# Performance work log

Hardware: AMD Instinct MI355X
Metric: run time of the kernel (lower is better)

## Reference

```python
import jax, jax.numpy as jnp
import numpy as np

B, C, H, W = 4, 128, 128, 128
E, K, HID = 11, 6, 512  # num_experts, active_experts, 4*dim


def setup_inputs() -> dict:
    key = jax.random.key(0)
    ks = jax.random.split(key, 5)
    return {
        "x": jax.random.normal(ks[0], (B, C, H, W), jnp.float32),
        "gate_w": jax.random.normal(ks[1], (E, C), jnp.float32) * 0.02,
        "gate_b": jnp.zeros((E,), jnp.float32),
        "w1": jax.random.normal(ks[2], (E, HID, C), jnp.float32) * 0.02,
        "b1": jnp.zeros((E, HID), jnp.float32),
        "w2": jax.random.normal(ks[3], (E, C, HID), jnp.float32) * 0.02,
        "b2": jnp.zeros((E, C), jnp.float32),
    }


def reference(x, gate_w, gate_b, w1, b1, w2, b2):
    n_experts = gate_w.shape[0]
    k = K  # active_experts
    # channels-last for per-pixel routing / 1x1-conv-as-matmul
    xcl = jnp.transpose(x, (0, 2, 3, 1))  # [B,H,W,C]
    # --- router (1x1 conv gate + softmax over experts + top-k) ---
    logits = jnp.einsum('bhwc,ec->bhwe', xcl, gate_w) + gate_b
    scores = jax.nn.softmax(logits, axis=-1)            # [B,H,W,E]
    topk_p, topk_i = jax.lax.top_k(scores, k)           # [B,H,W,K]
    topk_p = topk_p / topk_p.sum(axis=-1, keepdims=True)
    # scatter routing weights into dense per-expert mask (indices distinct)
    onehot = jax.nn.one_hot(topk_i, n_experts, dtype=x.dtype)  # [B,H,W,K,E]
    mask = jnp.einsum('bhwke,bhwk->bhwe', onehot, topk_p)      # [B,H,W,E]
    # --- dense expert compute, masked accumulate (as in original loop) ---
    acc = jnp.zeros_like(xcl)
    for e in range(n_experts):
        h = jax.nn.gelu(jnp.einsum('bhwc,dc->bhwd', xcl, w1[e]) + b1[e],
                        approximate=False)  # torch GELU is exact erf form
        oe = jnp.einsum('bhwd,cd->bhwc', h, w2[e]) + b2[e]
        acc = acc + mask[..., e:e + 1] * oe
    y = x + jnp.transpose(acc, (0, 3, 1, 2))  # back to NCHW
    # --- load-balancing aux loss ---
    mean_prob = scores.mean(axis=(0, 1, 2))            # [E]
    mean_load = onehot.sum(axis=3).mean(axis=(0, 1, 2))  # binary mask mean, [E]
    aux_loss = n_experts * jnp.sum(mean_prob * mean_load)
    return (y, aux_loss)
```

## Files before the change

kernel.cpp:

```cpp
#include <hip/hip_runtime.h>
#include <stdint.h>

#define C_   128
#define HW_  16384
#define CHW_ (C_*HW_)
#define N_   65536
#define E_   11
#define K_   6
#define HID_ 512

typedef __attribute__((ext_vector_type(8))) _Float16 half8;
typedef __attribute__((ext_vector_type(2))) _Float16 h2;
typedef __attribute__((ext_vector_type(2))) __fp16 fp16v2;
typedef __attribute__((ext_vector_type(16))) float float16v;
typedef __attribute__((ext_vector_type(2))) unsigned uint2v;

#define GLD(g, s) __builtin_amdgcn_global_load_lds( \
    (const __attribute__((address_space(1))) unsigned int*)(uintptr_t)(g), \
    (__attribute__((address_space(3))) unsigned int*)(unsigned int)(uintptr_t)(s), 16, 0, 0)

__device__ __forceinline__ h2 pkrtz(float a, float b){
  union { fp16v2 f; h2 h; } u;
  u.f = __builtin_amdgcn_cvt_pkrtz(a, b);
  return u.h;
}
__device__ __forceinline__ h2 gelu2h(h2 v, h2 wr2){
  h2 u = v * v;
  h2 s = u * (h2)(_Float16)(-0.00076957f) + (h2)(_Float16)(0.0147811f);
  s = s * u + (h2)(_Float16)(-0.126434f);
  s = s * u + (h2)(_Float16)(0.795742f);
  h2 p = v * s;
  h2 phi = p * (h2)(_Float16)(0.5f) + (h2)(_Float16)(0.5f);
  return v * wr2 * phi;
}
__device__ __forceinline__ void pswap32(unsigned &a, unsigned &b){
#if __has_builtin(__builtin_amdgcn_permlane32_swap)
  uint2v r = __builtin_amdgcn_permlane32_swap(a, b, false, false);
  a = r.x; b = r.y;
#else
  asm volatile("v_permlane32_swap_b32 %0, %1" : "+v"(a), "+v"(b));
#endif
}

__global__ __launch_bounds__(256) void k_prep(const float* __restrict__ x,
                                              const float* __restrict__ gw,
                                              const float* __restrict__ gb,
                                              const float* __restrict__ w1,
                                              const float* __restrict__ w2,
                                              const float* __restrict__ b1,
                                              unsigned short* __restrict__ xcl,
                                              float* __restrict__ mask,
                                              unsigned short* __restrict__ wimg,
                                              unsigned short* __restrict__ b1h,
                                              float* __restrict__ part){
  __shared__ __align__(16) float tt[64 * 130];
  __shared__ __align__(16) float g[E_ * C_];
  __shared__ float gbs[E_];
  __shared__ float ap[E_], al[E_];

  if (blockIdx.x < 726){
    int t = blockIdx.x * 256 + threadIdx.x;
    if (t >= 185856) return;
    if (t >= 180224){
      int t2 = t - 180224;
      int rec = t2 >> 5, j5 = t2 & 31;
      int hi = j5 >> 4, j = j5 & 15;
      int e = rec >> 4, hc = rec & 15;
      int row = (j & 3) + 8 * (j >> 2) + 4 * hi;
      union { _Float16 h; unsigned short u; } cv;
      cv.h = (_Float16)b1[e * 512 + hc * 32 + row];
      b1h[rec * 32 + j5] = cv.u;
      return;
    }
    const float* src;
    size_t dst;
    if (t < 90112){
      int e = t >> 13, hid = (t >> 4) & 511, c8 = t & 15;
      src = w1 + (size_t)t * 8;
      int rec = e * 16 + (hid >> 5);
      int kc = c8 >> 1, half = c8 & 1;
      int l = (hid & 31) | (half << 5);
      dst = (size_t)rec * 8192 + kc * 512 + l * 8;
    } else {
      int u = t - 90112;
      int e = u >> 13, cc = (u >> 6) & 127, hd8 = u & 63;
      src = w2 + (size_t)u * 8;
      int rec = e * 16 + (hd8 >> 2);
      int kc2 = (hd8 >> 1) & 1, half = hd8 & 1, ct = cc >> 5;
      int l = (cc & 31) | (half << 5);
      dst = (size_t)rec * 8192 + 4096 + (ct * 2 + kc2) * 512 + l * 8;
    }
    float4 a = *(const float4*)src, b = *(const float4*)(src + 4);
    union { _Float16 h[8]; uint4 v; } u4;
    u4.h[0] = (_Float16)a.x; u4.h[1] = (_Float16)a.y;
    u4.h[2] = (_Float16)a.z; u4.h[3] = (_Float16)a.w;
    u4.h[4] = (_Float16)b.x; u4.h[5] = (_Float16)b.y;
    u4.h[6] = (_Float16)b.z; u4.h[7] = (_Float16)b.w;
    *(uint4*)(wimg + dst) = u4.v;
    return;
  }

  int tid = threadIdx.x;
  int pb = blockIdx.x - 726;
  int pix0 = pb * 64;
  int b = pix0 >> 14, hw0 = pix0 & 16383;
  const float* xb = x + (size_t)b * CHW_ + hw0;

  for (int i = tid; i < E_ * C_; i += 256) g[i] = gw[i];
  if (tid < E_) { gbs[tid] = gb[tid]; ap[tid] = 0.f; al[tid] = 0.f; }

  #pragma unroll 4
  for (int it = 0; it < 32; ++it){
    int flat = it * 256 + tid;
    int c = flat >> 6, p = flat & 63;
    tt[p * 130 + c] = xb[c * HW_ + p];
  }
  __syncthreads();
  #pragma unroll 4
  for (int it = 0; it < 16; ++it){
    int u = it * 256 + tid;
    int p = u >> 6, cc = u & 63;
    float f0 = tt[p * 130 + 2 * cc], f1 = tt[p * 130 + 2 * cc + 1];
    union { h2 h; unsigned u; } pv;
    pv.h = pkrtz(f0, f1);
    ((unsigned*)xcl)[(size_t)(pix0 + p) * 64 + cc] = pv.u;
  }

  int p = tid >> 2, t4 = tid & 3;
  float lg[E_];
  #pragma unroll
  for (int e = 0; e < E_; ++e) lg[e] = (t4 == 0) ? gbs[e] : 0.f;
  const float2* ttrow = (const float2*)(tt + p * 130 + t4 * 32);
  #pragma unroll 4
  for (int j2 = 0; j2 < 16; ++j2){
    float2 xv = ttrow[j2];
    #pragma unroll
    for (int e = 0; e < E_; ++e){
      float2 gv = *(const float2*)(g + e * C_ + t4 * 32 + j2 * 2);
      lg[e] = fmaf(xv.x, gv.x, lg[e]);
      lg[e] = fmaf(xv.y, gv.y, lg[e]);
    }
  }
  #pragma unroll
  for (int e = 0; e < E_; ++e){
    lg[e] += __shfl_xor(lg[e], 1, 64);
    lg[e] += __shfl_xor(lg[e], 2, 64);
  }
  float mx = lg[0];
  #pragma unroll
  for (int e = 1; e < E_; ++e) mx = fmaxf(mx, lg[e]);
  float pr[E_]; float s = 0.f;
  #pragma unroll
  for (int e = 0; e < E_; ++e){ pr[e] = expf(lg[e] - mx); s += pr[e]; }
  float inv = 1.0f / s;
  #pragma unroll
  for (int e = 0; e < E_; ++e) pr[e] *= inv;

  unsigned selmask = 0; float wsum = 0.f;
  for (int k = 0; k < K_; ++k){
    float bv = -1.f; int bi = 0;
    #pragma unroll
    for (int e = 0; e < E_; ++e){
      bool better = (((selmask >> e) & 1u) == 0u) && (pr[e] > bv);
      bv = better ? pr[e] : bv;
      bi = better ? e : bi;
    }
    selmask |= 1u << bi; wsum += bv;
  }
  float invw = 1.0f / wsum;
  if (t4 == 0){
    int pix = pix0 + p;
    #pragma unroll
    for (int e = 0; e < E_; ++e){
      bool sel = (selmask >> e) & 1u;
      mask[(size_t)pix * E_ + e] = sel ? pr[e] * invw : 0.f;
      atomicAdd(&ap[e], pr[e]);
      if (sel) atomicAdd(&al[e], 1.0f);
    }
  }
  __syncthreads();
  if (tid < E_){
    part[tid * 1024 + pb]        = ap[tid];
    part[(E_ + tid) * 1024 + pb] = al[tid];
  }
}

__global__ __launch_bounds__(512, 2) void k_ffn(const unsigned short* __restrict__ xcl,
                                                const unsigned short* __restrict__ wimg,
                                                const unsigned short* __restrict__ b1h,
                                                const float* __restrict__ b2,
                                                const float* __restrict__ mask,
                                                const float* __restrict__ aux,
                                                const float* __restrict__ x,
                                                float* __restrict__ y){
  __shared__ unsigned char smem[65536];
  __shared__ int b2f;
  int tid = threadIdx.x;
  int w = tid >> 6, l = tid & 63;
  int l31 = l & 31, hi = l >> 5;
  int hi4 = hi * 4;
  int pix0 = blockIdx.x * 256;
  int off = (blockIdx.x % 11) * 16;
  const unsigned char* wimgB = (const unsigned char*)wimg;
  const unsigned char* b1hB  = (const unsigned char*)b1h;

  if (tid == 0) b2f = 0;

  if (blockIdx.x == 0 && w == 0){
    float s = 0.f;
    const float invN = 1.0f / (float)N_;
    for (int e = 0; e < E_; ++e){
      float pa = 0.f, pl = 0.f;
      #pragma unroll
      for (int i = 0; i < 16; ++i){
        pa += aux[e * 1024 + i * 64 + l];
        pl += aux[(E_ + e) * 1024 + i * 64 + l];
      }
      #pragma unroll
      for (int o = 32; o; o >>= 1){
        pa += __shfl_down(pa, o);
        pl += __shfl_down(pl, o);
      }
      if (l == 0) s += (pa * invN) * (pl * invN);
    }
    if (l == 0) y[(size_t)N_ * C_] = (float)E_ * s;
  }

  half8 Xf[8];
  {
    const unsigned short* xrow = xcl + ((size_t)(pix0 + w * 32 + l31) << 7) + hi * 8;
    #pragma unroll
    for (int kc = 0; kc < 8; ++kc)
      Xf[kc] = *(const half8*)(xrow + kc * 16);
  }

  uint4 bhA[4], bhB[4];
  const size_t mrow = (size_t)(pix0 + w * 32 + l31) * 11;

  {
    #pragma unroll
    for (int k = 0; k < 2; ++k){
      int rec = off + k;
      const unsigned char* gs = wimgB + (size_t)rec * 16384 + w * 2048 + l * 16;
      unsigned char* dst = smem + k * 16384 + w * 2048;
      GLD(gs, dst);
      GLD(gs + 1024, dst + 1024);
    }
    #pragma unroll
    for (int k = 0; k < 2; ++k){
      const unsigned char* bp = b1hB + (off + k) * 64 + hi * 32;
      bhA[2 * k]     = *(const uint4*)(bp);
      bhA[2 * k + 1] = *(const uint4*)(bp + 16);
    }
  }
  float wrn = mask[mrow + (off >> 4)];
  __syncthreads();

  float16v facc[4];
  #pragma unroll
  for (int ct = 0; ct < 4; ++ct) facc[ct] = (float16v)0.0f;
  h2 wr2 = (h2)(_Float16)0.0f;

#define REC_BODY(WB, BH0, BH1)                                                      \
  {                                                                                 \
    float16v hacc_ = (float16v)0.0f;                                                \
    _Pragma("unroll")                                                               \
    for (int kc_ = 0; kc_ < 8; ++kc_){                                              \
      half8 a_ = *(const half8*)((WB) + kc_ * 1024 + l * 16);                       \
      hacc_ = __builtin_amdgcn_mfma_f32_32x32x16_f16(a_, Xf[kc_], hacc_, 0, 0, 0);  \
    }                                                                               \
    union { uint4 v[2]; h2 h[8]; } bu_;                                             \
    bu_.v[0] = BH0; bu_.v[1] = BH1;                                                 \
    unsigned pd_[8];                                                                \
    _Pragma("unroll")                                                               \
    for (int k_ = 0; k_ < 8; ++k_){                                                 \
      h2 v_ = pkrtz(hacc_[2 * k_], hacc_[2 * k_ + 1]);                              \
      v_ = v_ + bu_.h[k_];                                                          \
      union { h2 h; unsigned u; } g_;                                               \
      g_.h = gelu2h(v_, wr2);                                                       \
      pd_[k_] = g_.u;                                                               \
    }                                                                               \
    pswap32(pd_[0], pd_[2]); pswap32(pd_[1], pd_[3]);                               \
    pswap32(pd_[4], pd_[6]); pswap32(pd_[5], pd_[7]);                               \
    union { unsigned u[4]; half8 s; } cv0_, cv1_;                                   \
    cv0_.u[0] = pd_[0]; cv0_.u[1] = pd_[1]; cv0_.u[2] = pd_[2]; cv0_.u[3] = pd_[3]; \
    cv1_.u[0] = pd_[4]; cv1_.u[1] = pd_[5]; cv1_.u[2] = pd_[6]; cv1_.u[3] = pd_[7]; \
    _Pragma("unroll")                                                               \
    for (int ct_ = 0; ct_ < 4; ++ct_){                                              \
      half8 a0_ = *(const half8*)((WB) + 8192 + (ct_ * 2 + 0) * 1024 + l * 16);     \
      half8 a1_ = *(const half8*)((WB) + 8192 + (ct_ * 2 + 1) * 1024 + l * 16);     \
      facc[ct_] = __builtin_amdgcn_mfma_f32_32x32x16_f16(a0_, cv0_.s, facc[ct_], 0, 0, 0); \
      facc[ct_] = __builtin_amdgcn_mfma_f32_32x32x16_f16(a1_, cv1_.s, facc[ct_], 0, 0, 0); \
    }                                                                               \
  }

#define SUPER_BODY(J, BHC, BHL)                                                     \
  {                                                                                 \
    asm volatile("s_waitcnt vmcnt(4)" ::: "memory");                                \
    __builtin_amdgcn_s_barrier();                                                   \
    __builtin_amdgcn_sched_barrier(0);                                              \
         \
    {                                                                               \
      unsigned char* dbuf_ = smem + ((((J) + 1) & 1) << 15);                        \
      _Pragma("unroll")                                                             \
      for (int k_ = 0; k_ < 2; ++k_){                                               \
        int rn_ = 2 * (J) + 2 + k_ + off; if (rn_ >= 176) rn_ -= 176;               \
        const unsigned char* gs_ = wimgB + (size_t)rn_ * 16384 + w * 2048 + l * 16; \
        unsigned char* dst_ = dbuf_ + k_ * 16384 + w * 2048;                        \
        GLD(gs_, dst_);                                                             \
        GLD(gs_ + 1024, dst_ + 1024);                                               \
      }                                                                             \
      __builtin_amdgcn_sched_barrier(0);                                            \
      _Pragma("unroll")                                                             \
      for (int k_ = 0; k_ < 2; ++k_){                                               \
        int rn_ = 2 * (J) + 2 + k_ + off; if (rn_ >= 176) rn_ -= 176;               \
        const unsigned char* bp_ = b1hB + rn_ * 64 + hi * 32;                       \
        BHL[2 * k_]     = *(const uint4*)(bp_);                                     \
        BHL[2 * k_ + 1] = *(const uint4*)(bp_ + 16);                                \
      }                                                                             \
    }                                                                               \
    __builtin_amdgcn_sched_barrier(0);                                              \
    if (((J) & 7) == 0){           \
      _Float16 wh_ = (_Float16)wrn;                                                 \
      wr2 = (h2){wh_, wh_};                                                         \
      int rn_ = 2 * (J) + 16 + off; if (rn_ >= 176) rn_ -= 176;                     \
      wrn = mask[mrow + (rn_ >> 4)];                                                \
    }                                                                               \
    const unsigned char* wb_ = smem + (((J) & 1) << 15);                            \
    REC_BODY(wb_, BHC[0], BHC[1]);                                                  \
    REC_BODY(wb_ + 16384, BHC[2], BHC[3]);                                          \
  }

  #pragma unroll 1
  for (int jj = 0; jj < 44; ++jj){
    SUPER_BODY(2 * jj,     bhA, bhB);
    SUPER_BODY(2 * jj + 1, bhB, bhA);
  }
#undef SUPER_BODY
#undef REC_BODY

  __syncthreads();
  float* lds_t = (float*)smem;
  float* b2t   = (float*)(smem + 17408);
  for (int idx = tid; idx < 1536; idx += 512){
    int cc = idx / 12, ee = idx - cc * 12;
    float v = (ee < 11) ? b2[ee * 128 + cc] : 0.f;
    b2t[idx] = v;
    if (v != 0.f) atomicOr(&b2f, 1);
  }
  __syncthreads();
  int b2nz = b2f;

  #pragma unroll 1
  for (int h = 0; h < 8; ++h){
    __syncthreads();
    if (w == h){
      #pragma unroll
      for (int ct = 0; ct < 4; ++ct)
        #pragma unroll
        for (int r = 0; r < 16; ++r)
          lds_t[(ct * 32 + (r & 3) + 8 * (r >> 2) + hi4) * 33 + l31] = facc[ct][r];
    }
    __syncthreads();
    int c = tid >> 2, p8 = (tid & 3) << 3;
    int pixg = pix0 + h * 32 + p8;
    size_t base = (size_t)(pixg >> 14) * CHW_ + (size_t)c * HW_ + (pixg & 16383);
    float av[8];
    #pragma unroll
    for (int k = 0; k < 8; ++k) av[k] = lds_t[c * 33 + p8 + k];
    if (b2nz){
      #pragma unroll
      for (int k = 0; k < 8; ++k){
        const float* mr = mask + (size_t)(pixg + k) * 11;
        #pragma unroll
        for (int e = 0; e < 11; ++e) av[k] = fmaf(mr[e], b2t[c * 12 + e], av[k]);
      }
    }
    float4 xv0 = *(const float4*)(x + base);
    float4 xv1 = *(const float4*)(x + base + 4);
    float4 o0 = {av[0] + xv0.x, av[1] + xv0.y, av[2] + xv0.z, av[3] + xv0.w};
    float4 o1 = {av[4] + xv1.x, av[5] + xv1.y, av[6] + xv1.z, av[7] + xv1.w};
    *(float4*)(y + base) = o0;
    *(float4*)(y + base + 4) = o1;
  }
}

extern "C" void kernel_launch(void* const* d_in, const int* in_sizes, int n_in,
                              void* d_out, int out_size, void* d_ws, size_t ws_size,
                              hipStream_t stream){
  const float* x  = (const float*)d_in[0];
  const float* gw = (const float*)d_in[1];
  const float* gb = (const float*)d_in[2];
  const float* w1 = (const float*)d_in[3];
  const float* b1 = (const float*)d_in[4];
  const float* w2 = (const float*)d_in[5];
  const float* b2 = (const float*)d_in[6];
  float* y = (float*)d_out;
  char* ws = (char*)d_ws;

  unsigned short* xcl  = (unsigned short*)ws;
  unsigned short* wimg = (unsigned short*)(ws + 16777216);
  float* mask   = (float*)(ws + 19660800);
  float* part   = (float*)(ws + 22544384);
  unsigned short* b1h  = (unsigned short*)(ws + 22634496);

  hipLaunchKernelGGL(k_prep, dim3(1750), dim3(256), 0, stream,
                     x, gw, gb, w1, w2, b1, xcl, mask, wimg, b1h, part);
  hipLaunchKernelGGL(k_ffn,  dim3(256),  dim3(512), 0, stream,
                     xcl, wimg, b1h, b2, mask, part, x, y);
}
```

Baseline: 308.8 us.

## Fuse router and x transpose into FFN kernel; split weight conversion and aux

Result: slower. 330.5 us (+7.0%).

```diff
diff --git a/kernel.cpp b/kernel.cpp
--- a/kernel.cpp
+++ b/kernel.cpp
@@ -42,156 +42,62 @@
 #endif
 }
 
-__global__ __launch_bounds__(256) void k_prep(const float* __restrict__ x,
-                                              const float* __restrict__ gw,
-                                              const float* __restrict__ gb,
-                                              const float* __restrict__ w1,
-                                              const float* __restrict__ w2,
-                                              const float* __restrict__ b1,
-                                              unsigned short* __restrict__ xcl,
-                                              float* __restrict__ mask,
-                                              unsigned short* __restrict__ wimg,
-                                              unsigned short* __restrict__ b1h,
-                                              float* __restrict__ part){
-  __shared__ __align__(16) float tt[64 * 130];
-  __shared__ __align__(16) float g[E_ * C_];
-  __shared__ float gbs[E_];
-  __shared__ float ap[E_], al[E_];
-
-  if (blockIdx.x < 726){
-    int t = blockIdx.x * 256 + threadIdx.x;
-    if (t >= 185856) return;
-    if (t >= 180224){
-      int t2 = t - 180224;
-      int rec = t2 >> 5, j5 = t2 & 31;
-      int hi = j5 >> 4, j = j5 & 15;
-      int e = rec >> 4, hc = rec & 15;
-      int row = (j & 3) + 8 * (j >> 2) + 4 * hi;
-      union { _Float16 h; unsigned short u; } cv;
-      cv.h = (_Float16)b1[e * 512 + hc * 32 + row];
-      b1h[rec * 32 + j5] = cv.u;
-      return;
-    }
-    const float* src;
-    size_t dst;
-    if (t < 90112){
-      int e = t >> 13, hid = (t >> 4) & 511, c8 = t & 15;
-      src = w1 + (size_t)t * 8;
-      int rec = e * 16 + (hid >> 5);
-      int kc = c8 >> 1, half = c8 & 1;
-      int l = (hid & 31) | (half << 5);
-      dst = (size_t)rec * 8192 + kc * 512 + l * 8;
-    } else {
-      int u = t - 90112;
-      int e = u >> 13, cc = (u >> 6) & 127, hd8 = u & 63;
-      src = w2 + (size_t)u * 8;
-      int rec = e * 16 + (hd8 >> 2);
-      int kc2 = (hd8 >> 1) & 1, half = hd8 & 1, ct = cc >> 5;
-      int l = (cc & 31) | (half << 5);
-      dst = (size_t)rec * 8192 + 4096 + (ct * 2 + kc2) * 512 + l * 8;
-    }
-    float4 a = *(const float4*)src, b = *(const float4*)(src + 4);
-    union { _Float16 h[8]; uint4 v; } u4;
-    u4.h[0] = (_Float16)a.x; u4.h[1] = (_Float16)a.y;
-    u4.h[2] = (_Float16)a.z; u4.h[3] = (_Float16)a.w;
-    u4.h[4] = (_Float16)b.x; u4.h[5] = (_Float16)b.y;
-    u4.h[6] = (_Float16)b.z; u4.h[7] = (_Float16)b.w;
-    *(uint4*)(wimg + dst) = u4.v;
+__global__ __launch_bounds__(256) void k_convert(const float* __restrict__ w1,
+                                                 const float* __restrict__ w2,
+                                                 const float* __restrict__ b1,
+                                                 unsigned short* __restrict__ wimg,
+                                                 unsigned short* __restrict__ b1h,
+                                                 float* __restrict__ auxsum){
+  int t = blockIdx.x * 256 + threadIdx.x;
+  if (t < 23) auxsum[t] = 0.0f;
+  if (t >= 185856) return;
+  if (t >= 180224){
+    int t2 = t - 180224;
+    int rec = t2 >> 5, j5 = t2 & 31;
+    int hi = j5 >> 4, j = j5 & 15;
+    int e = rec >> 4, hc = rec & 15;
+    int row = (j & 3) + 8 * (j >> 2) + 4 * hi;
+    union { _Float16 h; unsigned short u; } cv;
+    cv.h = (_Float16)b1[e * 512 + hc * 32 + row];
+    b1h[rec * 32 + j5] = cv.u;
     return;
   }
-
-  int tid = threadIdx.x;
-  int pb = blockIdx.x - 726;
-  int pix0 = pb * 64;
-  int b = pix0 >> 14, hw0 = pix0 & 16383;
-  const float* xb = x + (size_t)b * CHW_ + hw0;
-
-  for (int i = tid; i < E_ * C_; i += 256) g[i] = gw[i];
-  if (tid < E_) { gbs[tid] = gb[tid]; ap[tid] = 0.f; al[tid] = 0.f; }
-
-  #pragma unroll 4
-  for (int it = 0; it < 32; ++it){
-    int flat = it * 256 + tid;
-    int c = flat >> 6, p = flat & 63;
-    tt[p * 130 + c] = xb[c * HW_ + p];
-  }
-  __syncthreads();
-  #pragma unroll 4
-  for (int it = 0; it < 16; ++it){
-    int u = it * 256 + tid;
-    int p = u >> 6, cc = u & 63;
-    float f0 = tt[p * 130 + 2 * cc], f1 = tt[p * 130 + 2 * cc + 1];
-    union { h2 h; unsigned u; } pv;
-    pv.h = pkrtz(f0, f1);
-    ((unsigned*)xcl)[(size_t)(pix0 + p) * 64 + cc] = pv.u;
-  }
-
-  int p = tid >> 2, t4 = tid & 3;
-  float lg[E_];
-  #pragma unroll
-  for (int e = 0; e < E_; ++e) lg[e] = (t4 == 0) ? gbs[e] : 0.f;
-  const float2* ttrow = (const float2*)(tt + p * 130 + t4 * 32);
-  #pragma unroll 4
-  for (int j2 = 0; j2 < 16; ++j2){
-    float2 xv = ttrow[j2];
-    #pragma unroll
-    for (int e = 0; e < E_; ++e){
-      float2 gv = *(const float2*)(g + e * C_ + t4 * 32 + j2 * 2);
-      lg[e] = fmaf(xv.x, gv.x, lg[e]);
-      lg[e] = fmaf(xv.y, gv.y, lg[e]);
-    }
-  }
-  #pragma unroll
-  for (int e = 0; e < E_; ++e){
-    lg[e] += __shfl_xor(lg[e], 1, 64);
-    lg[e] += __shfl_xor(lg[e], 2, 64);
-  }
-  float mx = lg[0];
-  #pragma unroll
-  for (int e = 1; e < E_; ++e) mx = fmaxf(mx, lg[e]);
-  float pr[E_]; float s = 0.f;
-  #pragma unroll
-  for (int e = 0; e < E_; ++e){ pr[e] = expf(lg[e] - mx); s += pr[e]; }
-  float inv = 1.0f / s;
-  #pragma unroll
-  for (int e = 0; e < E_; ++e) pr[e] *= inv;
-
-  unsigned selmask = 0; float wsum = 0.f;
-  for (int k = 0; k < K_; ++k){
-    float bv = -1.f; int bi = 0;
-    #pragma unroll
-    for (int e = 0; e < E_; ++e){
-      bool better = (((selmask >> e) & 1u) == 0u) && (pr[e] > bv);
-      bv = better ? pr[e] : bv;
-      bi = better ? e : bi;
-    }
-    selmask |= 1u << bi; wsum += bv;
-  }
-  float invw = 1.0f / wsum;
-  if (t4 == 0){
-    int pix = pix0 + p;
-    #pragma unroll
-    for (int e = 0; e < E_; ++e){
-      bool sel = (selmask >> e) & 1u;
-      mask[(size_t)pix * E_ + e] = sel ? pr[e] * invw : 0.f;
-      atomicAdd(&ap[e], pr[e]);
-      if (sel) atomicAdd(&al[e], 1.0f);
-    }
-  }
-  __syncthreads();
-  if (tid < E_){
-    part[tid * 1024 + pb]        = ap[tid];
-    part[(E_ + tid) * 1024 + pb] = al[tid];
-  }
-}
-
-__global__ __launch_bounds__(512, 2) void k_ffn(const unsigned short* __restrict__ xcl,
+  const float* src;
+  size_t dst;
+  if (t < 90112){
+    int e = t >> 13, hid = (t >> 4) & 511, c8 = t & 15;
+    src = w1 + (size_t)t * 8;
+    int rec = e * 16 + (hid >> 5);
+    int kc = c8 >> 1, half = c8 & 1;
+    int l = (hid & 31) | (half << 5);
+    dst = (size_t)rec * 8192 + kc * 512 + l * 8;
+  } else {
+    int u = t - 90112;
+    int e = u >> 13, cc = (u >> 6) & 127, hd8 = u & 63;
+    src = w2 + (size_t)u * 8;
+    int rec = e * 16 + (hd8 >> 2);
+    int kc2 = (hd8 >> 1) & 1, half = hd8 & 1, ct = cc >> 5;
+    int l = (cc & 31) | (half << 5);
+    dst = (size_t)rec * 8192 + 4096 + (ct * 2 + kc2) * 512 + l * 8;
+  }
+  float4 a = *(const float4*)src, b = *(const float4*)(src + 4);
+  union { _Float16 h[8]; uint4 v; } u4;
+  u4.h[0] = (_Float16)a.x; u4.h[1] = (_Float16)a.y;
+  u4.h[2] = (_Float16)a.z; u4.h[3] = (_Float16)a.w;
+  u4.h[4] = (_Float16)b.x; u4.h[5] = (_Float16)b.y;
+  u4.h[6] = (_Float16)b.z; u4.h[7] = (_Float16)b.w;
+  *(uint4*)(wimg + dst) = u4.v;
+}
+
+__global__ __launch_bounds__(512, 2) void k_ffn(const float* __restrict__ x,
+                                                const float* __restrict__ gw,
+                                                const float* __restrict__ gb,
+                                                unsigned short* __restrict__ xcl,
+                                                float* __restrict__ mask,
                                                 const unsigned short* __restrict__ wimg,
                                                 const unsigned short* __restrict__ b1h,
                                                 const float* __restrict__ b2,
-                                                const float* __restrict__ mask,
-                                                const float* __restrict__ aux,
-                                                const float* __restrict__ x,
+                                                float* __restrict__ auxsum,
                                                 float* __restrict__ y){
   __shared__ unsigned char smem[65536];
   __shared__ int b2f;
@@ -206,24 +112,96 @@
 
   if (tid == 0) b2f = 0;
 
-  if (blockIdx.x == 0 && w == 0){
-    float s = 0.f;
-    const float invN = 1.0f / (float)N_;
-    for (int e = 0; e < E_; ++e){
-      float pa = 0.f, pl = 0.f;
+  {
+    float* tt  = (float*)smem;
+    float* g   = (float*)(smem + 33280);
+    float* gbs = (float*)(smem + 38912);
+    float* ap  = (float*)(smem + 38976);
+    float* al  = (float*)(smem + 39040);
+
+    for (int i = tid; i < E_ * C_; i += 512) g[i] = gw[i];
+    if (tid < E_){ gbs[tid] = gb[tid]; ap[tid] = 0.f; al[tid] = 0.f; }
+
+    #pragma unroll 1
+    for (int rr = 0; rr < 4; ++rr){
+      int pixc = pix0 + rr * 64;
+      const float* xb = x + (size_t)(pixc >> 14) * CHW_ + (pixc & 16383);
+      __syncthreads();
       #pragma unroll
-      for (int i = 0; i < 16; ++i){
-        pa += aux[e * 1024 + i * 64 + l];
-        pl += aux[(E_ + e) * 1024 + i * 64 + l];
+      for (int it = 0; it < 16; ++it){
+        int flat = it * 512 + tid;
+        int c = flat >> 6, p = flat & 63;
+        tt[p * 130 + c] = xb[(size_t)c * HW_ + p];
       }
+      __syncthreads();
       #pragma unroll
-      for (int o = 32; o; o >>= 1){
-        pa += __shfl_down(pa, o);
-        pl += __shfl_down(pl, o);
+      for (int it = 0; it < 8; ++it){
+        int u = it * 512 + tid;
+        int p = u >> 6, cc = u & 63;
+        union { h2 h; unsigned u32; } pv;
+        pv.h = pkrtz(tt[p * 130 + 2 * cc], tt[p * 130 + 2 * cc + 1]);
+        ((unsigned*)xcl)[(size_t)(pixc + p) * 64 + cc] = pv.u32;
       }
-      if (l == 0) s += (pa * invN) * (pl * invN);
-    }
-    if (l == 0) y[(size_t)N_ * C_] = (float)E_ * s;
+      if (tid < 256){
+        int p = tid >> 2, t4 = tid & 3;
+        float lg[E_];
+        #pragma unroll
+        for (int e = 0; e < E_; ++e) lg[e] = (t4 == 0) ? gbs[e] : 0.f;
+        const float2* ttrow = (const float2*)(tt + p * 130 + t4 * 32);
+        #pragma unroll 4
+        for (int j2 = 0; j2 < 16; ++j2){
+          float2 xv = ttrow[j2];
+          #pragma unroll
+          for (int e = 0; e < E_; ++e){
+            float2 gv = *(const float2*)(g + e * C_ + t4 * 32 + j2 * 2);
+            lg[e] = fmaf(xv.x, gv.x, lg[e]);
+            lg[e] = fmaf(xv.y, gv.y, lg[e]);
+          }
+        }
+        #pragma unroll
+        for (int e = 0; e < E_; ++e){
+          lg[e] += __shfl_xor(lg[e], 1, 64);
+          lg[e] += __shfl_xor(lg[e], 2, 64);
+        }
+        float mx = lg[0];
+        #pragma unroll
+        for (int e = 1; e < E_; ++e) mx = fmaxf(mx, lg[e]);
+        float pr[E_]; float s = 0.f;
+        #pragma unroll
+        for (int e = 0; e < E_; ++e){ pr[e] = expf(lg[e] - mx); s += pr[e]; }
+        float inv = 1.0f / s;
+        #pragma unroll
+        for (int e = 0; e < E_; ++e) pr[e] *= inv;
+
+        unsigned selmask = 0; float wsum = 0.f;
+        for (int k = 0; k < K_; ++k){
+          float bv = -1.f; int bi = 0;
+          #pragma unroll
+          for (int e = 0; e < E_; ++e){
+            bool better = (((selmask >> e) & 1u) == 0u) && (pr[e] > bv);
+            bv = better ? pr[e] : bv;
+            bi = better ? e : bi;
+          }
+          selmask |= 1u << bi; wsum += bv;
+        }
+        float invw = 1.0f / wsum;
+        if (t4 == 0){
+          int pix = pixc + p;
+          #pragma unroll
+          for (int e = 0; e < E_; ++e){
+            bool sel = (selmask >> e) & 1u;
+            mask[(size_t)pix * E_ + e] = sel ? pr[e] * invw : 0.f;
+            atomicAdd(&ap[e], pr[e]);
+            if (sel) atomicAdd(&al[e], 1.0f);
+          }
+        }
+      }
+    }
+    __syncthreads();
+    if (tid < E_){
+      atomicAdd(&auxsum[tid], ap[tid]);
+      atomicAdd(&auxsum[E_ + tid], al[tid]);
+    }
   }
 
   half8 Xf[8];
@@ -385,6 +363,17 @@
   }
 }
 
+__global__ __launch_bounds__(64) void k_aux(const float* __restrict__ aux,
+                                            float* __restrict__ y){
+  if (threadIdx.x == 0){
+    float s = 0.f;
+    const float invN = 1.0f / (float)N_;
+    for (int e = 0; e < E_; ++e)
+      s += (aux[e] * invN) * (aux[E_ + e] * invN);
+    y[(size_t)N_ * C_] = (float)E_ * s;
+  }
+}
+
 extern "C" void kernel_launch(void* const* d_in, const int* in_sizes, int n_in,
                               void* d_out, int out_size, void* d_ws, size_t ws_size,
                               hipStream_t stream){
@@ -401,11 +390,11 @@
   unsigned short* xcl  = (unsigned short*)ws;
   unsigned short* wimg = (unsigned short*)(ws + 16777216);
   float* mask   = (float*)(ws + 19660800);
-  float* part   = (float*)(ws + 22544384);
-  unsigned short* b1h  = (unsigned short*)(ws + 22634496);
-
-  hipLaunchKernelGGL(k_prep, dim3(1750), dim3(256), 0, stream,
-                     x, gw, gb, w1, w2, b1, xcl, mask, wimg, b1h, part);
-  hipLaunchKernelGGL(k_ffn,  dim3(256),  dim3(512), 0, stream,
-                     xcl, wimg, b1h, b2, mask, part, x, y);
-}
+  float* auxsum = (float*)(ws + 22544384);
+  unsigned short* b1h  = (unsigned short*)(ws + 22544480);
+
+  hipLaunchKernelGGL(k_convert, dim3(726), dim3(256), 0, stream, w1, w2, b1, wimg, b1h, auxsum);
+  hipLaunchKernelGGL(k_ffn,     dim3(256), dim3(512), 0, stream,
+                     x, gw, gb, xcl, mask, wimg, b1h, b2, auxsum, y);
+  hipLaunchKernelGGL(k_aux,     dim3(1),   dim3(64),  0, stream, auxsum, y);
+}
```
